# Performance work log

Measured on AMD Instinct MI355X. Metric: run time of the kernel, lower is better.

Reference implementation:

```python
import jax, jax.numpy as jnp
import numpy as np

EXPAND = 2
KCONV = 4


def _mamba(x, Win, Wconv, bconv, Wx, Wdt, bdt, Alog, Dskip, Wout):
    # x: (B, C, H, W) -> flatten HW to a sequence, run Mamba (S6) block, reshape back
    B, C, H, W = x.shape
    L = H * W
    Di, Kc = Wconv.shape
    R = Wdt.shape[0]
    N = Alog.shape[1]
    xl = x.reshape(B, C, L).transpose(0, 2, 1)            # (B, L, C)
    xz = xl @ Win                                          # (B, L, 2*Di)
    xs, z = xz[..., :Di], xz[..., Di:]
    xt = xs.transpose(0, 2, 1)                             # (B, Di, L)
    xp = jnp.pad(xt, ((0, 0), (0, 0), (Kc - 1, 0)))        # causal depthwise conv1d
    conv = bconv[None, :, None]
    for k in range(Kc):
        conv = conv + Wconv[:, k][None, :, None] * xp[:, :, k:k + L]
    u = jax.nn.silu(conv).transpose(0, 2, 1)               # (B, L, Di)
    dbc = u @ Wx                                           # (B, L, R+2N)
    dt = jax.nn.softplus(dbc[..., :R] @ Wdt + bdt)         # (B, L, Di)
    Bm = dbc[..., R:R + N]                                 # (B, L, N)
    Cm = dbc[..., R + N:]                                  # (B, L, N)
    A = -jnp.exp(Alog)                                     # (Di, N)
    dA = jnp.exp(dt[..., None] * A)                        # (B, L, Di, N)
    dBx = dt[..., None] * Bm[:, :, None, :] * u[..., None] # (B, L, Di, N)

    def step(h, inp):
        a, bx, c = inp
        h = a * h + bx
        return h, jnp.einsum('bdn,bn->bd', h, c)

    h0 = jnp.zeros((B, Di, N), x.dtype)
    _, ys = jax.lax.scan(step, h0, (jnp.swapaxes(dA, 0, 1), jnp.swapaxes(dBx, 0, 1), jnp.swapaxes(Cm, 0, 1)))
    y = jnp.swapaxes(ys, 0, 1) + u * Dskip                 # (B, L, Di)
    y = y * jax.nn.silu(z)
    return (y @ Wout).transpose(0, 2, 1).reshape(B, C, H, W)


def _resize_bilinear(x, oh, ow):
    # F.interpolate(mode='bilinear', align_corners=True)
    B, C, H, W = x.shape
    ys = jnp.linspace(0.0, H - 1.0, oh)
    xs = jnp.linspace(0.0, W - 1.0, ow)
    y0 = jnp.floor(ys).astype(jnp.int32); y1 = jnp.clip(y0 + 1, 0, H - 1); wy = (ys - y0)[:, None]
    x0 = jnp.floor(xs).astype(jnp.int32); x1 = jnp.clip(x0 + 1, 0, W - 1); wx = (xs - x0)[None, :]
    r0 = x[:, :, y0, :]
    r1 = x[:, :, y1, :]
    top = r0[..., x0] * (1 - wx) + r0[..., x1] * wx
    bot = r1[..., x0] * (1 - wx) + r1[..., x1] * wx
    return top * (1 - wy) + bot * wy


def _mamba_params(key, D, N):
    Di = EXPAND * D
    R = max(1, D // 16)
    ks = jax.random.split(key, 6)
    s = 0.02
    Win = s * jax.random.normal(ks[0], (D, 2 * Di), jnp.float32)
    Wconv = s * jax.random.normal(ks[1], (Di, KCONV), jnp.float32)
    bconv = jnp.zeros((Di,), jnp.float32)
    Wx = s * jax.random.normal(ks[2], (Di, R + 2 * N), jnp.float32)
    Wdt = s * jax.random.normal(ks[3], (R, Di), jnp.float32)
    bdt = s * jax.random.normal(ks[4], (Di,), jnp.float32)
    Alog = jnp.tile(jnp.log(jnp.arange(1, N + 1, dtype=jnp.float32))[None, :], (Di, 1))
    Dskip = jnp.ones((Di,), jnp.float32)
    Wout = s * jax.random.normal(ks[5], (Di, D), jnp.float32)
    return Win, Wconv, bconv, Wx, Wdt, bdt, Alog, Dskip, Wout


def setup_inputs() -> dict:
    key = jax.random.key(0)
    C, B, N = 64, 2, 16
    sizes = [48, 24, 12, 6]
    ks = jax.random.split(key, 16)
    inp = {}
    for i, s in enumerate(sizes):
        inp[f'feat{i}'] = jax.random.normal(ks[i], (B, C, s, s), jnp.float32)
    names = ['Win', 'Wconv', 'bconv', 'Wx', 'Wdt', 'bdt', 'Alog', 'D', 'Wout']
    lvl = [_mamba_params(ks[4 + i], C, N) for i in range(4)]
    for j, nm in enumerate(names):
        inp['lvl_' + nm] = jnp.stack([lvl[i][j] for i in range(4)])
    cr = _mamba_params(ks[8], 4 * C, N)
    for j, nm in enumerate(names):
        inp['cr_' + nm] = cr[j]
    inp['proj_W'] = 0.02 * jax.random.normal(ks[9], (C, 4 * C), jnp.float32)  # 1x1 conv weight (out,in)
    inp['proj_b'] = jnp.zeros((C,), jnp.float32)
    inp['bn_g'] = jnp.ones((C,), jnp.float32)
    inp['bn_b'] = jnp.zeros((C,), jnp.float32)
    inp['bn_m'] = 0.1 * jax.random.normal(ks[10], (C,), jnp.float32)
    inp['bn_v'] = jax.random.uniform(ks[11], (C,), jnp.float32, minval=0.5, maxval=1.5)
    inp['target_h'] = 48
    inp['target_w'] = 48
    return inp


def reference(feat0, feat1, feat2, feat3,
              lvl_Win, lvl_Wconv, lvl_bconv, lvl_Wx, lvl_Wdt, lvl_bdt, lvl_Alog, lvl_D, lvl_Wout,
              cr_Win, cr_Wconv, cr_bconv, cr_Wx, cr_Wdt, cr_bdt, cr_Alog, cr_D, cr_Wout,
              proj_W, proj_b, bn_g, bn_b, bn_m, bn_v, target_h, target_w):
    feats = [feat0, feat1, feat2, feat3]
    processed = []
    for i, f in enumerate(feats):
        f = f + _mamba(f, lvl_Win[i], lvl_Wconv[i], lvl_bconv[i], lvl_Wx[i], lvl_Wdt[i],
                       lvl_bdt[i], lvl_Alog[i], lvl_D[i], lvl_Wout[i])
        processed.append(_resize_bilinear(f, target_h, target_w))
    x = jnp.concatenate(processed, axis=1)                 # (B, 4C, th, tw)
    x = x + _mamba(x, cr_Win, cr_Wconv, cr_bconv, cr_Wx, cr_Wdt, cr_bdt, cr_Alog, cr_D, cr_Wout)
    y = jnp.einsum('bchw,oc->bohw', x, proj_W) + proj_b[None, :, None, None]
    scale = (bn_g / jnp.sqrt(bn_v + 1e-5))[None, :, None, None]
    y = (y - bn_m[None, :, None, None]) * scale + bn_b[None, :, None, None]
    return jax.nn.relu(y)
```

## Files before the change

### kernel.cpp

```cpp
#include <hip/hip_runtime.h>
#include <cmath>

#define DEV __device__ __forceinline__

typedef unsigned short u16;
typedef u16 u16x8 __attribute__((ext_vector_type(8)));
typedef u16 u16x4 __attribute__((ext_vector_type(4)));
typedef short bf16x8 __attribute__((ext_vector_type(8)));
typedef float f32x4 __attribute__((ext_vector_type(4)));

constexpr int B_ = 2;
constexpr int S4[4]    = {48, 24, 12, 6};
constexpr int L4[4]    = {2304, 576, 144, 36};
constexpr int LOFF4[4] = {0, 2304, 2880, 3024};
constexpr int LTOT = 3060;
constexpr int TOFF4[4] = {0, 144, 180, 189};
constexpr int NTT = 192;
constexpr int NCH4[4]   = {36, 9, 3, 1};
constexpr int CHOFF4[4] = {0, 36, 45, 48};
constexpr int NCHL = 49;
constexpr int NCHC = 36;
constexpr int LC = 2304;
constexpr float LOG2E = 1.44269504088896f;

DEV float siluf(float x) { return x / (1.f + __expf(-x)); }
DEV float softplusf(float x) { return fmaxf(x, 0.f) + log1pf(__expf(-fabsf(x))); }
DEV float b2f(u16 x) { union { float f; unsigned u; } v; v.u = ((unsigned)x) << 16; return v.f; }
DEV u16 f2b(float f) {
  union { float f; unsigned u; } v; v.f = f;
  unsigned r = v.u + 0x7fffu + ((v.u >> 16) & 1u);
  return (u16)(r >> 16);
}

__global__ __launch_bounds__(256) void k_prep(
    const float* __restrict__ projW, const float* __restrict__ crWout,
    const float* __restrict__ cWin, const float* __restrict__ cWx,
    float* __restrict__ Wt, float* __restrict__ WP,
    u16* __restrict__ WinT, float* __restrict__ WxT) {
  __shared__ float sm[64 * 65];
  int blk = blockIdx.x;
  int tid = threadIdx.x;
  if (blk < 64) {
    int i = blk * 256 + tid;
    int o = i >> 8, c = i & 255;
    Wt[c * 64 + o] = projW[o * 256 + c];
  } else if (blk < 192) {
    int i = (blk - 64) * 256 + tid;
    int d = i >> 6, o = i & 63;
    float acc = 0.f;
#pragma unroll 4
    for (int c = 0; c < 256; ++c)
      acc = fmaf(crWout[d * 256 + c], projW[o * 256 + c], acc);
    WP[d * 64 + o] = acc;
  } else if (blk < 256) {
    int t = blk - 192;
    int ct = t & 3, nt = t >> 2;
    int c0 = ct * 64, n0 = nt * 64;
    for (int i = tid; i < 4096; i += 256) {
      int cc = i >> 6, nn = i & 63;
      sm[cc * 65 + nn] = cWin[(size_t)(c0 + cc) * 1024 + n0 + nn];
    }
    __syncthreads();
    for (int i = tid; i < 4096; i += 256) {
      int nn = i >> 6, cc = i & 63;
      WinT[(size_t)(n0 + nn) * 256 + c0 + cc] = f2b(sm[cc * 65 + nn]);
    }
  } else {
    int i = (blk - 256) * 256 + tid;
    int d = i & 511, j = i >> 9;
    WxT[j * 512 + d] = cWx[d * 48 + j];
  }
}

__global__ __launch_bounds__(256) void k_front_lvl(
    const float* __restrict__ f0, const float* __restrict__ f1,
    const float* __restrict__ f2, const float* __restrict__ f3,
    const float* __restrict__ Win,
    const float* __restrict__ Wconv,
    const float* __restrict__ bconv,
    const float* __restrict__ Wx,
    const float* __restrict__ Wdt,
    const float* __restrict__ bdt,
    u16* __restrict__ u_l, u16* __restrict__ dt_l,
    u16* __restrict__ Bm_l, u16* __restrict__ Cm_l, u16* __restrict__ z_l) {
  __shared__ float s_x[64 * 20];
  __shared__ float s_xs[19 * 128];
  __shared__ float s_u[16 * 132];
  __shared__ float s_dbc[16 * 36];
  int bid = blockIdx.x;
  int b = bid / NTT, t = bid - b * NTT;
  int lvl = 0;
  while (lvl < 3 && t >= TOFF4[lvl + 1]) ++lvl;
  int tl = t - TOFF4[lvl];
  int L = L4[lvl], loff = LOFF4[lvl];
  int l0 = tl * 16;
  int nl = min(16, L - l0);
  const float* fx = lvl == 0 ? f0 : lvl == 1 ? f1 : lvl == 2 ? f2 : f3;
  int tid = threadIdx.x;

  for (int i = tid; i < 64 * 20; i += 256) {
    int c = i / 20, r = i - c * 20;
    int l = l0 - 3 + r;
    float v = 0.f;
    if (r < 19 && l >= 0 && l < L) v = fx[(size_t)(b * 64 + c) * L + l];
    s_x[i] = v;
  }
  __syncthreads();
  {
    int j = tid;
    float acc[19];
#pragma unroll
    for (int r = 0; r < 19; ++r) acc[r] = 0.f;
    const float* W = Win + lvl * 64 * 256 + j;
    for (int c = 0; c < 64; ++c) {
      float w = W[c * 256];
#pragma unroll
      for (int r = 0; r < 19; ++r) acc[r] = fmaf(w, s_x[c * 20 + r], acc[r]);
    }
    if (j < 128) {
#pragma unroll
      for (int r = 0; r < 19; ++r) s_xs[r * 128 + j] = acc[r];
    } else {
      int d = j - 128;
      int dti = d >> 4, jj = d & 15;
      for (int r = 3; r < 19; ++r) {
        int l = l0 - 3 + r;
        if (l < l0 + nl)
          z_l[((size_t)(b * 8 + dti) * LTOT + loff + l) * 16 + jj] = f2b(acc[r]);
      }
    }
  }
  __syncthreads();
  for (int i = tid; i < 16 * 128; i += 256) {
    int l = i >> 7, d = i & 127;
    if (l < nl) {
      const float* wc = Wconv + (lvl * 128 + d) * 4;
      float a = bconv[lvl * 128 + d];
#pragma unroll
      for (int k = 0; k < 4; ++k) a = fmaf(wc[k], s_xs[(l + k) * 128 + d], a);
      float uu = siluf(a);
      s_u[l * 132 + d] = uu;
      u_l[((size_t)(b * 8 + (d >> 4)) * LTOT + loff + l0 + l) * 16 + (d & 15)] = f2b(uu);
    }
  }
  __syncthreads();
  for (int i = tid; i < 16 * 36; i += 256) {
    int l = i & 15, jj = i >> 4;
    if (l < nl) {
      const float* wx = Wx + lvl * 128 * 36 + jj;
      float a = 0.f;
      for (int d = 0; d < 128; ++d) a = fmaf(s_u[l * 132 + d], wx[d * 36], a);
      s_dbc[l * 36 + jj] = a;
      if (jj >= 4) {
        int q = jj - 4;
        size_t gb = ((size_t)(b * LTOT) + loff + l0 + l) * 16;
        if (q < 16) Bm_l[gb + q] = f2b(a);
        else        Cm_l[gb + (q - 16)] = f2b(a);
      }
    }
  }
  __syncthreads();
  for (int i = tid; i < 16 * 128; i += 256) {
    int l = i >> 7, d = i & 127;
    if (l < nl) {
      float a = bdt[lvl * 128 + d];
#pragma unroll
      for (int r = 0; r < 4; ++r)
        a = fmaf(s_dbc[l * 36 + r], Wdt[(lvl * 4 + r) * 128 + d], a);
      dt_l[((size_t)(b * 8 + (d >> 4)) * LTOT + loff + l0 + l) * 16 + (d & 15)] =
          f2b(softplusf(a));
    }
  }
}

template <int MODE, int PASSC>
__global__ __launch_bounds__(256) void k_scan(
    const u16* __restrict__ dtb, const u16* __restrict__ ub,
    const u16* __restrict__ Bmb, const u16* __restrict__ Cmb,
    const u16* __restrict__ zb,
    const float* __restrict__ Alog, const float* __restrict__ Dsk,
    float* __restrict__ hloc, float* __restrict__ Ssum,
    const float* __restrict__ hin, u16* __restrict__ yg) {
  constexpr int DI = MODE ? 512 : 128;
  constexpr int NDT = DI / 16;
  constexpr int NB = DI / 64;
  constexpr int NCHT = MODE ? NCHC : NCHL;
  constexpr int LT = MODE ? LC : LTOT;
  __shared__ __align__(16) u16 smem[PASSC ? 14336 : 9216];
  u16* s_dt = smem;
  u16* s_u  = smem + 4096;
  u16* s_B  = smem + 8192;
  u16* s_C  = PASSC ? smem + 9216 : nullptr;
  u16* s_y  = PASSC ? smem + 10240 : nullptr;

  int bid = blockIdx.x;
  int dblk = bid % NB;
  int rem = bid / NB;
  int gc = rem % NCHT;
  int b = rem / NCHT;
  int lvl = 0, ch = gc, Lq = LC, loff = 0;
  if (MODE == 0) {
    while (lvl < 3 && gc >= CHOFF4[lvl + 1]) ++lvl;
    ch = gc - CHOFF4[lvl];
    Lq = L4[lvl];
    loff = LOFF4[lvl];
  }
  int l0 = ch * 64;
  int len = min(64, Lq - l0);
  int labs0 = loff + l0;
  int tid = threadIdx.x;
  int q = tid & 3;
  int dl = (tid >> 2) & 15;
  int ti_l = tid >> 6;
  int dti = dblk * 4 + ti_l;
  int d = dti * 16 + dl;
  int n0 = q * 4;

  for (int ti = 0; ti < 4; ++ti) {
    size_t g2 = ((size_t)(b * NDT + dblk * 4 + ti) * LT + labs0) * 16;
    const u16x8* pdt = (const u16x8*)(dtb + g2);
    const u16x8* pu  = (const u16x8*)(ub + g2);
    for (int i = tid; i < len * 2; i += 256) {
      *(u16x8*)&s_dt[ti * 1024 + i * 8] = pdt[i];
      *(u16x8*)&s_u [ti * 1024 + i * 8] = pu[i];
    }
  }
  {
    size_t gB = ((size_t)b * LT + labs0) * 16;
    for (int i = tid; i < len * 2; i += 256) {
      *(u16x8*)&s_B[i * 8] = *(const u16x8*)&Bmb[gB + i * 8];
      if (PASSC) *(u16x8*)&s_C[i * 8] = *(const u16x8*)&Cmb[gB + i * 8];
    }
  }
  __syncthreads();

  int ai = (MODE ? d : lvl * 128 + d);
  float4 al = *(const float4*)&Alog[ai * 16 + n0];
  float kA2[4] = {-__expf(al.x) * LOG2E, -__expf(al.y) * LOG2E,
                  -__expf(al.z) * LOG2E, -__expf(al.w) * LOG2E};
  size_t hix = (((size_t)(b * NCHT) + gc) * DI + d) * 16 + n0;
  float h[4] = {0.f, 0.f, 0.f, 0.f};
  if (PASSC) {
    float4 hv = *(const float4*)&hin[hix];
    h[0] = hv.x; h[1] = hv.y; h[2] = hv.z; h[3] = hv.w;
  }
  float dsk = PASSC ? Dsk[ai] : 0.f;
  float ss = 0.f;

  for (int l = 0; l < len; ++l) {
    float dt = b2f(s_dt[ti_l * 1024 + l * 16 + dl]);
    float uu = b2f(s_u [ti_l * 1024 + l * 16 + dl]);
    float dtu = dt * uu;
    u16x4 Bv = *(const u16x4*)&s_B[l * 16 + n0];
    if (PASSC) {
      u16x4 Cv = *(const u16x4*)&s_C[l * 16 + n0];
      float p = 0.f;
#pragma unroll
      for (int i = 0; i < 4; ++i) {
        float dA = exp2f(kA2[i] * dt);
        h[i] = fmaf(dA, h[i], dtu * b2f(Bv[i]));
        p = fmaf(h[i], b2f(Cv[i]), p);
      }
      p += __shfl_xor(p, 1, 4);
      p += __shfl_xor(p, 2, 4);
      if (q == 0) s_y[l * 64 + ti_l * 16 + dl] = f2b(fmaf(uu, dsk, p));
    } else {
#pragma unroll
      for (int i = 0; i < 4; ++i) {
        float dA = exp2f(kA2[i] * dt);
        h[i] = fmaf(dA, h[i], dtu * b2f(Bv[i]));
      }
      ss += dt;
    }
  }
  if (!PASSC) {
    f32x4 hv = {h[0], h[1], h[2], h[3]};
    *(f32x4*)&hloc[hix] = hv;
    if (q == 0) Ssum[((size_t)(b * NCHT) + gc) * DI + d] = ss;
  } else {
    __syncthreads();
    for (int ti = 0; ti < 4; ++ti) {
      size_t g2 = ((size_t)(b * NDT + dblk * 4 + ti) * LT + labs0) * 16;
      for (int i = tid; i < len * 2; i += 256) {
        u16x8 zv = *(const u16x8*)&zb[g2 + i * 8];
        u16x8 yv = *(const u16x8*)&s_y[(i >> 1) * 64 + ti * 16 + (i & 1) * 8];
        u16x8 o;
#pragma unroll
        for (int j = 0; j < 8; ++j) {
          float z = b2f(zv[j]);
          float gate = z / (1.f + __expf(-z));
          o[j] = f2b(b2f(yv[j]) * gate);
        }
        *(u16x8*)&yg[g2 + i * 8] = o;
      }
    }
  }
}

__global__ __launch_bounds__(256) void k_combine_lvl(
    const float* __restrict__ Alog, const float* __restrict__ hloc,
    const float* __restrict__ Ssum, float* __restrict__ hin) {
  int i = blockIdx.x * 256 + threadIdx.x;
  int n = i & 15, d = (i >> 4) & 127, lvl = (i >> 11) & 3, b = i >> 13;
  float kA2 = -__expf(Alog[(lvl * 128 + d) * 16 + n]) * LOG2E;
  float h = 0.f;
  int nch = NCH4[lvl];
  for (int ch = 0; ch < nch; ++ch) {
    int gc = CHOFF4[lvl] + ch;
    size_t ix = (((size_t)(b * NCHL) + gc) * 128 + d) * 16 + n;
    hin[ix] = h;
    float S = Ssum[((size_t)(b * NCHL) + gc) * 128 + d];
    h = fmaf(exp2f(kA2 * S), h, hloc[ix]);
  }
}

__global__ __launch_bounds__(256) void k_combine_cr(
    const float* __restrict__ Alog, const float* __restrict__ hloc,
    const float* __restrict__ Ssum, float* __restrict__ hin) {
  int i = blockIdx.x * 256 + threadIdx.x;
  int n = i & 15, d = (i >> 4) & 511, b = i >> 13;
  float kA2 = -__expf(Alog[d * 16 + n]) * LOG2E;
  float h = 0.f;
  for (int ch = 0; ch < NCHC; ++ch) {
    size_t ix = (((size_t)(b * NCHC) + ch) * 512 + d) * 16 + n;
    hin[ix] = h;
    float S = Ssum[((size_t)(b * NCHC) + ch) * 512 + d];
    h = fmaf(exp2f(kA2 * S), h, hloc[ix]);
  }
}

__global__ __launch_bounds__(256) void k_out_lvl(
    const u16* __restrict__ yg_l, const float* __restrict__ Wout,
    const float* __restrict__ f0, const float* __restrict__ f1,
    const float* __restrict__ f2, const float* __restrict__ f3,
    float* __restrict__ fout) {
  __shared__ float s_ygT[128 * 20];
  __shared__ float s_o[16 * 64];
  int bid = blockIdx.x;
  int b = bid / NTT, t = bid - b * NTT;
  int lvl = 0;
  while (lvl < 3 && t >= TOFF4[lvl + 1]) ++lvl;
  int tl = t - TOFF4[lvl];
  int L = L4[lvl], loff = LOFF4[lvl];
  int l0 = tl * 16, nl = min(16, L - l0);
  const float* fx = lvl == 0 ? f0 : lvl == 1 ? f1 : lvl == 2 ? f2 : f3;
  int tid = threadIdx.x;
  for (int i = tid; i < 16 * 128; i += 256) {
    int d = i & 127, l = i >> 7;
    float v = 0.f;
    if (l < nl)
      v = b2f(yg_l[((size_t)(b * 8 + (d >> 4)) * LTOT + loff + l0 + l) * 16 + (d & 15)]);
    s_ygT[d * 20 + l] = v;
  }
  __syncthreads();
  {
    int c = tid & 63, lg = (tid >> 6) * 4;
    float acc[4] = {0.f, 0.f, 0.f, 0.f};
    const float* W = Wout + lvl * 128 * 64 + c;
    for (int dq = 0; dq < 128; ++dq) {
      float w = W[dq * 64];
      float4 yv = *(const float4*)&s_ygT[dq * 20 + lg];
      acc[0] = fmaf(w, yv.x, acc[0]);
      acc[1] = fmaf(w, yv.y, acc[1]);
      acc[2] = fmaf(w, yv.z, acc[2]);
      acc[3] = fmaf(w, yv.w, acc[3]);
    }
#pragma unroll
    for (int a = 0; a < 4; ++a) s_o[(lg + a) * 64 + c] = acc[a];
  }
  __syncthreads();
  for (int i = tid; i < 16 * 64; i += 256) {
    int c = i >> 4, l = i & 15;
    if (l < nl)
      fout[((size_t)(b * 64) + c) * LTOT + loff + l0 + l] =
          s_o[l * 64 + c] + fx[((size_t)(b * 64) + c) * L + l0 + l];
  }
}

__global__ __launch_bounds__(256) void k_resize(const float* __restrict__ fout,
                                                float* __restrict__ xTf,
                                                u16* __restrict__ xTb) {
  int i = blockIdx.x * 256 + threadIdx.x;
  int ch = i & 255;
  int rem = i >> 8;
  int hw = rem % 2304;
  int b = rem / 2304;
  int oh = hw / 48, ow = hw - oh * 48;
  int lvl = ch >> 6, c = ch & 63;
  int s = S4[lvl];
  const float* base = fout + ((size_t)(b * 64) + c) * LTOT + LOFF4[lvl];
  float scl = (float)(s - 1) * (1.f / 47.f);
  float fy = oh * scl, fxx = ow * scl;
  int y0 = (int)floorf(fy), x0 = (int)floorf(fxx);
  float wy = fy - y0, wx = fxx - x0;
  int y1 = min(y0 + 1, s - 1), x1 = min(x0 + 1, s - 1);
  float v00 = base[y0 * s + x0], v01 = base[y0 * s + x1];
  float v10 = base[y1 * s + x0], v11 = base[y1 * s + x1];
  float top = v00 * (1.f - wx) + v01 * wx;
  float bot = v10 * (1.f - wx) + v11 * wx;
  float v = top * (1.f - wy) + bot * wy;
  xTf[i] = v;
  xTb[i] = f2b(v);
}

__global__ __launch_bounds__(256) void k_gemm_mfma(
    const u16* __restrict__ xT,
    const u16* __restrict__ WT,
    u16* __restrict__ xs_c, u16* __restrict__ z_c) {
  __shared__ __align__(16) u16 s_a[64 * 72];
  __shared__ __align__(16) u16 s_b[128 * 72];
  int bid = blockIdx.x;
  int nj = bid & 7, bm = bid >> 3;
  int tid = threadIdx.x;
  int lane = tid & 63, w = tid >> 6;
  int wm = (w & 1) * 32, wn = (w >> 1) * 64;
  const int m_base = bm * 64;
  const int n_base = nj * 128;

  f32x4 acc[2][4];
#pragma unroll
  for (int mi = 0; mi < 2; ++mi)
#pragma unroll
    for (int ni = 0; ni < 4; ++ni) acc[mi][ni] = {0.f, 0.f, 0.f, 0.f};

  u16x8 ra0, ra1, rb0, rb1, rb2, rb3;
  auto ld = [&](int c0) {
#pragma unroll
    for (int s = 0; s < 2; ++s) {
      int v = s * 256 + tid;
      int row = v >> 3, kc = (v & 7) * 8;
      u16x8 t = *(const u16x8*)&xT[(size_t)(m_base + row) * 256 + c0 + kc];
      if (s == 0) ra0 = t; else ra1 = t;
    }
#pragma unroll
    for (int s = 0; s < 4; ++s) {
      int v = s * 256 + tid;
      int row = v >> 3, kc = (v & 7) * 8;
      u16x8 t = *(const u16x8*)&WT[(size_t)(n_base + row) * 256 + c0 + kc];
      if (s == 0) rb0 = t; else if (s == 1) rb1 = t;
      else if (s == 2) rb2 = t; else rb3 = t;
    }
  };
  auto st = [&]() {
#pragma unroll
    for (int s = 0; s < 2; ++s) {
      int v = s * 256 + tid;
      int row = v >> 3, kc = (v & 7) * 8;
      *(u16x8*)&s_a[row * 72 + kc] = (s == 0) ? ra0 : ra1;
    }
#pragma unroll
    for (int s = 0; s < 4; ++s) {
      int v = s * 256 + tid;
      int row = v >> 3, kc = (v & 7) * 8;
      const u16x8& t = (s == 0) ? rb0 : (s == 1) ? rb1 : (s == 2) ? rb2 : rb3;
      *(u16x8*)&s_b[row * 72 + kc] = t;
    }
  };
  ld(0);
  int mlane = lane & 15, kg = (lane >> 4) * 8;
  for (int kt = 0; kt < 4; ++kt) {
    st();
    __syncthreads();
    if (kt < 3) ld((kt + 1) * 64);
#pragma unroll
    for (int kk = 0; kk < 2; ++kk) {
      int k0 = kk * 32 + kg;
      bf16x8 af[2], bfr[4];
#pragma unroll
      for (int mi = 0; mi < 2; ++mi)
        af[mi] = *(const bf16x8*)&s_a[(wm + mi * 16 + mlane) * 72 + k0];
#pragma unroll
      for (int ni = 0; ni < 4; ++ni)
        bfr[ni] = *(const bf16x8*)&s_b[(wn + ni * 16 + mlane) * 72 + k0];
#pragma unroll
      for (int mi = 0; mi < 2; ++mi)
#pragma unroll
        for (int ni = 0; ni < 4; ++ni)
          acc[mi][ni] = __builtin_amdgcn_mfma_f32_16x16x32_bf16(
              af[mi], bfr[ni], acc[mi][ni], 0, 0, 0);
    }
    __syncthreads();
  }
  int rgrp = (lane >> 4) * 4;
#pragma unroll
  for (int mi = 0; mi < 2; ++mi) {
#pragma unroll
    for (int ni = 0; ni < 4; ++ni) {
      int n = n_base + wn + ni * 16 + mlane;
#pragma unroll
      for (int r = 0; r < 4; ++r) {
        int gm = m_base + wm + mi * 16 + rgrp + r;
        int b = gm >= 2304;
        int l = gm - b * 2304;
        u16 v = f2b(acc[mi][ni][r]);
        if (n < 512) {
          xs_c[((size_t)(b * LC) + l) * 512 + n] = v;
        } else {
          int dz = n - 512;
          z_c[((size_t)(b * 32 + (dz >> 4)) * LC + l) * 16 + (dz & 15)] = v;
        }
      }
    }
  }
}

__global__ __launch_bounds__(256) void k_mid_cr(
    const u16* __restrict__ xs_c,
    const float* __restrict__ Wconv,
    const float* __restrict__ bconv,
    const float* __restrict__ WxT,
    const float* __restrict__ Wdt,
    const float* __restrict__ bdt, u16* __restrict__ u_c,
    u16* __restrict__ dt_c, u16* __restrict__ Bm_c, u16* __restrict__ Cm_c) {
  __shared__ __align__(16) u16 s_xs[11 * 512];
  __shared__ __align__(16) float s_u[8 * 516];
  __shared__ float s_dbc[8 * 48];
  int bid = blockIdx.x;
  int b = bid / 288, tl = bid - b * 288;
  int l0 = tl * 8;
  int tid = threadIdx.x;
  for (int i = tid; i < 704; i += 256) {
    int r = i >> 6;
    int l = l0 - 3 + r;
    u16x8 v = {0, 0, 0, 0, 0, 0, 0, 0};
    if (l >= 0)
      v = *(const u16x8*)&xs_c[((size_t)(b * LC) + l) * 512 + (i & 63) * 8];
    *(u16x8*)&s_xs[i * 8] = v;
  }
  __syncthreads();
  for (int i = tid; i < 8 * 512; i += 256) {
    int l = i >> 9, d = i & 511;
    const float* wc = Wconv + d * 4;
    float a = bconv[d];
#pragma unroll
    for (int k = 0; k < 4; ++k) a = fmaf(wc[k], b2f(s_xs[(l + k) * 512 + d]), a);
    float uu = siluf(a);
    s_u[l * 516 + d] = uu;
    u_c[((size_t)(b * 32 + (d >> 4)) * LC + l0 + l) * 16 + (d & 15)] = f2b(uu);
  }
  __syncthreads();
  for (int i = tid; i < 8 * 48; i += 256) {
    int jj = i >> 3, l = i & 7;
    const float* wx = WxT + jj * 512;
    float a = 0.f;
#pragma unroll 4
    for (int d = 0; d < 512; d += 4) {
      float4 w4 = *(const float4*)&wx[d];
      float4 u4 = *(const float4*)&s_u[l * 516 + d];
      a = fmaf(w4.x, u4.x, a);
      a = fmaf(w4.y, u4.y, a);
      a = fmaf(w4.z, u4.z, a);
      a = fmaf(w4.w, u4.w, a);
    }
    s_dbc[l * 48 + jj] = a;
    if (jj >= 16) {
      int q = jj - 16;
      size_t gb = ((size_t)(b * LC) + l0 + l) * 16;
      if (q < 16) Bm_c[gb + q] = f2b(a);
      else        Cm_c[gb + (q - 16)] = f2b(a);
    }
  }
  __syncthreads();
  for (int i = tid; i < 8 * 512; i += 256) {
    int l = i >> 9, d = i & 511;
    float a = bdt[d];
#pragma unroll
    for (int r = 0; r < 16; ++r)
      a = fmaf(s_dbc[l * 48 + r], Wdt[r * 512 + d], a);
    dt_c[((size_t)(b * 32 + (d >> 4)) * LC + l0 + l) * 16 + (d & 15)] =
        f2b(softplusf(a));
  }
}

__global__ __launch_bounds__(256) void k_final(
    const float* __restrict__ xTf, const u16* __restrict__ yg_c,
    const float* __restrict__ Wt, const float* __restrict__ WP,
    const float* __restrict__ pb, const float* __restrict__ bng,
    const float* __restrict__ bnb, const float* __restrict__ bnm,
    const float* __restrict__ bnv, float* __restrict__ out) {
  __shared__ float s_xc[256 * 8];
  __shared__ float s_yg[512 * 8];
  __shared__ float s_w[32 * 64];
  int bid = blockIdx.x;
  int b = bid / 288, tl = bid - b * 288;
  int l0 = tl * 8;
  int tid = threadIdx.x;
  for (int i = tid; i < 2048; i += 256) {
    int c = i & 255, l = i >> 8;
    s_xc[c * 8 + l] = xTf[((size_t)(b * 2304) + l0 + l) * 256 + c];
  }
  for (int i = tid; i < 4096; i += 256) {
    int j = i & 15, l = (i >> 4) & 7, dt = i >> 7;
    s_yg[(dt * 16 + j) * 8 + l] =
        b2f(yg_c[((size_t)(b * 32 + dt) * LC + l0 + l) * 16 + j]);
  }
  int o = tid & 63, lg = (tid >> 6) * 2;
  float acc0 = 0.f, acc1 = 0.f;
  float4 r0, r1;
  auto ldT = [&](const float* W, int kt, float4& a0, float4& a1) {
#pragma unroll
    for (int s = 0; s < 2; ++s) {
      int idx = s * 256 + tid;
      int row = idx >> 4, c4 = (idx & 15) << 2;
      float4 v = *(const float4*)&W[(kt * 32 + row) * 64 + c4];
      if (s == 0) a0 = v; else a1 = v;
    }
  };
  auto stT = [&](const float4& a0, const float4& a1) {
#pragma unroll
    for (int s = 0; s < 2; ++s) {
      int idx = s * 256 + tid;
      int row = idx >> 4, c4 = (idx & 15) << 2;
      *(float4*)&s_w[row * 64 + c4] = (s == 0) ? a0 : a1;
    }
  };
  ldT(Wt, 0, r0, r1);
  __syncthreads();
  stT(r0, r1);
  __syncthreads();
  for (int kt = 0; kt < 8; ++kt) {
    if (kt < 7) ldT(Wt, kt + 1, r0, r1);
    else ldT(WP, 0, r0, r1);
#pragma unroll
    for (int cc = 0; cc < 32; ++cc) {
      float w = s_w[cc * 64 + o];
      float2 xv = *(const float2*)&s_xc[(kt * 32 + cc) * 8 + lg];
      acc0 = fmaf(w, xv.x, acc0);
      acc1 = fmaf(w, xv.y, acc1);
    }
    __syncthreads();
    stT(r0, r1);
    __syncthreads();
  }
  for (int kt = 0; kt < 16; ++kt) {
    if (kt < 15) ldT(WP, kt + 1, r0, r1);
#pragma unroll
    for (int cc = 0; cc < 32; ++cc) {
      float w = s_w[cc * 64 + o];
      float2 yv = *(const float2*)&s_yg[(kt * 32 + cc) * 8 + lg];
      acc0 = fmaf(w, yv.x, acc0);
      acc1 = fmaf(w, yv.y, acc1);
    }
    __syncthreads();
    if (kt < 15) {
      stT(r0, r1);
      __syncthreads();
    }
  }
  float bias = pb[o], m = bnm[o], g = bng[o], v = bnv[o], bb = bnb[o];
  float scl = g * (1.f / sqrtf(v + 1e-5f));
  float2 r;
  r.x = fmaxf((acc0 + bias - m) * scl + bb, 0.f);
  r.y = fmaxf((acc1 + bias - m) * scl + bb, 0.f);
  *(float2*)&out[((size_t)(b * 64) + o) * LC + l0 + lg] = r;
}

extern "C" void kernel_launch(void* const* d_in, const int* in_sizes, int n_in,
                              void* d_out, int out_size, void* d_ws,
                              size_t ws_size, hipStream_t stream) {
  (void)in_sizes; (void)n_in; (void)out_size; (void)ws_size;
  const float* f0 = (const float*)d_in[0];
  const float* f1 = (const float*)d_in[1];
  const float* f2 = (const float*)d_in[2];
  const float* f3 = (const float*)d_in[3];
  const float* lWin   = (const float*)d_in[4];
  const float* lWconv = (const float*)d_in[5];
  const float* lbconv = (const float*)d_in[6];
  const float* lWx    = (const float*)d_in[7];
  const float* lWdt   = (const float*)d_in[8];
  const float* lbdt   = (const float*)d_in[9];
  const float* lAlog  = (const float*)d_in[10];
  const float* lD     = (const float*)d_in[11];
  const float* lWout  = (const float*)d_in[12];
  const float* cWin   = (const float*)d_in[13];
  const float* cWconv = (const float*)d_in[14];
  const float* cbconv = (const float*)d_in[15];
  const float* cWx    = (const float*)d_in[16];
  const float* cWdt   = (const float*)d_in[17];
  const float* cbdt   = (const float*)d_in[18];
  const float* cAlog  = (const float*)d_in[19];
  const float* cD     = (const float*)d_in[20];
  const float* cWout  = (const float*)d_in[21];
  const float* projW  = (const float*)d_in[22];
  const float* projb  = (const float*)d_in[23];
  const float* bng    = (const float*)d_in[24];
  const float* bnb    = (const float*)d_in[25];
  const float* bnm    = (const float*)d_in[26];
  const float* bnv    = (const float*)d_in[27];
  float* out = (float*)d_out;

  float* ws = (float*)d_ws;
  size_t off = 0;
  auto allocf = [&](size_t n) { float* p = ws + off; off += (n + 7) & ~(size_t)7; return p; };
  auto allocb = [&](size_t n) { u16* p = (u16*)(ws + off); off += ((n + 1) / 2 + 7) & ~(size_t)7; return p; };

  float* Wt     = allocf(256 * 64);
  float* WP     = allocf(512 * 64);
  float* WxT    = allocf(48 * 512);
  float* fout   = allocf((size_t)B_ * 64 * LTOT);
  float* xTf    = allocf((size_t)B_ * LC * 256);
  float* hloc_l = allocf((size_t)B_ * NCHL * 128 * 16);
  float* S_l    = allocf((size_t)B_ * NCHL * 128);
  float* hin_l  = allocf((size_t)B_ * NCHL * 128 * 16);
  float* hloc_c = allocf((size_t)B_ * NCHC * 512 * 16);
  float* S_c    = allocf((size_t)B_ * NCHC * 512);
  float* hin_c  = allocf((size_t)B_ * NCHC * 512 * 16);

  u16* WinT  = allocb(1024 * 256);
  u16* xTb   = allocb((size_t)B_ * LC * 256);
  u16* u_l2  = allocb((size_t)B_ * 8 * LTOT * 16);
  u16* dt_l2 = allocb((size_t)B_ * 8 * LTOT * 16);
  u16* z_l2  = allocb((size_t)B_ * 8 * LTOT * 16);
  u16* yg_l2 = allocb((size_t)B_ * 8 * LTOT * 16);
  u16* Bm_l2 = allocb((size_t)B_ * LTOT * 16);
  u16* Cm_l2 = allocb((size_t)B_ * LTOT * 16);
  u16* xs_c2 = allocb((size_t)B_ * LC * 512);
  u16* u_c2  = allocb((size_t)B_ * 32 * LC * 16);
  u16* dt_c2 = allocb((size_t)B_ * 32 * LC * 16);
  u16* z_c2  = allocb((size_t)B_ * 32 * LC * 16);
  u16* yg_c2 = allocb((size_t)B_ * 32 * LC * 16);
  u16* Bm_c2 = allocb((size_t)B_ * LC * 16);
  u16* Cm_c2 = allocb((size_t)B_ * LC * 16);

  k_prep<<<352, 256, 0, stream>>>(projW, cWout, cWin, cWx, Wt, WP, WinT, WxT);

  k_front_lvl<<<B_ * NTT, 256, 0, stream>>>(f0, f1, f2, f3, lWin, lWconv,
                                            lbconv, lWx, lWdt, lbdt, u_l2,
                                            dt_l2, Bm_l2, Cm_l2, z_l2);

  k_scan<0, 0><<<B_ * NCHL * 2, 256, 0, stream>>>(
      dt_l2, u_l2, Bm_l2, Cm_l2, nullptr, lAlog, lD, hloc_l, S_l, nullptr,
      nullptr);
  k_combine_lvl<<<64, 256, 0, stream>>>(lAlog, hloc_l, S_l, hin_l);
  k_scan<0, 1><<<B_ * NCHL * 2, 256, 0, stream>>>(
      dt_l2, u_l2, Bm_l2, Cm_l2, z_l2, lAlog, lD, nullptr, nullptr, hin_l,
      yg_l2);

  k_out_lvl<<<B_ * NTT, 256, 0, stream>>>(yg_l2, lWout, f0, f1, f2, f3, fout);
  k_resize<<<(B_ * 256 * LC) / 256, 256, 0, stream>>>(fout, xTf, xTb);

  k_gemm_mfma<<<72 * 8, 256, 0, stream>>>(xTb, WinT, xs_c2, z_c2);
  k_mid_cr<<<B_ * 288, 256, 0, stream>>>(xs_c2, cWconv, cbconv, WxT, cWdt,
                                         cbdt, u_c2, dt_c2, Bm_c2, Cm_c2);

  k_scan<1, 0><<<B_ * NCHC * 8, 256, 0, stream>>>(
      dt_c2, u_c2, Bm_c2, Cm_c2, nullptr, cAlog, cD, hloc_c, S_c, nullptr,
      nullptr);
  k_combine_cr<<<64, 256, 0, stream>>>(cAlog, hloc_c, S_c, hin_c);
  k_scan<1, 1><<<B_ * NCHC * 8, 256, 0, stream>>>(
      dt_c2, u_c2, Bm_c2, Cm_c2, z_c2, cAlog, cD, nullptr, nullptr, hin_c,
      yg_c2);

  k_final<<<B_ * 288, 256, 0, stream>>>(xTf, yg_c2, Wt, WP, projb, bng, bnb,
                                        bnm, bnv, out);
}
```

Baseline: 350.6 us.

## Retile cross-level mid kernel: 16 positions per block, LDS-staged Wx projection

```diff
diff --git a/kernel.cpp b/kernel.cpp
--- a/kernel.cpp
+++ b/kernel.cpp
@@ -504,7 +504,7 @@
   }
 }
 
-__global__ __launch_bounds__(256) void k_mid_cr(
+__global__ __launch_bounds__(1024) void k_mid_cr(
     const u16* __restrict__ xs_c,
     const float* __restrict__ Wconv,
     const float* __restrict__ bconv,
@@ -512,56 +512,76 @@
     const float* __restrict__ Wdt,
     const float* __restrict__ bdt, u16* __restrict__ u_c,
     u16* __restrict__ dt_c, u16* __restrict__ Bm_c, u16* __restrict__ Cm_c) {
-  __shared__ __align__(16) u16 s_xs[11 * 512];
-  __shared__ __align__(16) float s_u[8 * 516];
-  __shared__ float s_dbc[8 * 48];
+  __shared__ __align__(16) u16 s_xs[19 * 512];
+  __shared__ __align__(16) u16 s_ub[16 * 520];
+  __shared__ __align__(16) float s_wx[48 * 132];
+  __shared__ float s_dbc[16 * 48];
   int bid = blockIdx.x;
-  int b = bid / 288, tl = bid - b * 288;
-  int l0 = tl * 8;
+  int b = bid / 144, tl = bid - b * 144;
+  int l0 = tl * 16;
   int tid = threadIdx.x;
-  for (int i = tid; i < 704; i += 256) {
-    int r = i >> 6;
+  for (int i = tid; i < 19 * 64; i += 1024) {
+    int r = i >> 6, c8 = (i & 63) * 8;
     int l = l0 - 3 + r;
     u16x8 v = {0, 0, 0, 0, 0, 0, 0, 0};
     if (l >= 0)
-      v = *(const u16x8*)&xs_c[((size_t)(b * LC) + l) * 512 + (i & 63) * 8];
-    *(u16x8*)&s_xs[i * 8] = v;
-  }
-  __syncthreads();
-  for (int i = tid; i < 8 * 512; i += 256) {
+      v = *(const u16x8*)&xs_c[((size_t)(b * LC) + l) * 512 + c8];
+    *(u16x8*)&s_xs[r * 512 + c8] = v;
+  }
+  __syncthreads();
+  for (int i = tid; i < 16 * 512; i += 1024) {
     int l = i >> 9, d = i & 511;
     const float* wc = Wconv + d * 4;
     float a = bconv[d];
 #pragma unroll
     for (int k = 0; k < 4; ++k) a = fmaf(wc[k], b2f(s_xs[(l + k) * 512 + d]), a);
     float uu = siluf(a);
-    s_u[l * 516 + d] = uu;
-    u_c[((size_t)(b * 32 + (d >> 4)) * LC + l0 + l) * 16 + (d & 15)] = f2b(uu);
-  }
-  __syncthreads();
-  for (int i = tid; i < 8 * 48; i += 256) {
-    int jj = i >> 3, l = i & 7;
-    const float* wx = WxT + jj * 512;
-    float a = 0.f;
+    u16 ub = f2b(uu);
+    s_ub[l * 520 + d] = ub;
+    u_c[((size_t)(b * 32 + (d >> 4)) * LC + l0 + l) * 16 + (d & 15)] = ub;
+  }
+  int dl = tid & 15, jj = tid >> 4;
+  float a8[8] = {0.f, 0.f, 0.f, 0.f, 0.f, 0.f, 0.f, 0.f};
+  for (int kt = 0; kt < 4; ++kt) {
+    __syncthreads();
+    for (int i = tid; i < 1536; i += 1024) {
+      int row = i >> 5, c4 = (i & 31) * 4;
+      *(float4*)&s_wx[row * 132 + c4] =
+          *(const float4*)&WxT[row * 512 + kt * 128 + c4];
+    }
+    __syncthreads();
+    if (tid < 768) {
+      const u16* ur = s_ub + dl * 520 + kt * 128;
+      const float* wr = s_wx + jj * 132;
 #pragma unroll 4
-    for (int d = 0; d < 512; d += 4) {
-      float4 w4 = *(const float4*)&wx[d];
-      float4 u4 = *(const float4*)&s_u[l * 516 + d];
-      a = fmaf(w4.x, u4.x, a);
-      a = fmaf(w4.y, u4.y, a);
-      a = fmaf(w4.z, u4.z, a);
-      a = fmaf(w4.w, u4.w, a);
-    }
-    s_dbc[l * 48 + jj] = a;
+      for (int kb = 0; kb < 16; ++kb) {
+        u16x8 uv = *(const u16x8*)&ur[kb * 8];
+        float4 w0 = *(const float4*)&wr[kb * 8];
+        float4 w1 = *(const float4*)&wr[kb * 8 + 4];
+        a8[0] = fmaf(b2f(uv[0]), w0.x, a8[0]);
+        a8[1] = fmaf(b2f(uv[1]), w0.y, a8[1]);
+        a8[2] = fmaf(b2f(uv[2]), w0.z, a8[2]);
+        a8[3] = fmaf(b2f(uv[3]), w0.w, a8[3]);
+        a8[4] = fmaf(b2f(uv[4]), w1.x, a8[4]);
+        a8[5] = fmaf(b2f(uv[5]), w1.y, a8[5]);
+        a8[6] = fmaf(b2f(uv[6]), w1.z, a8[6]);
+        a8[7] = fmaf(b2f(uv[7]), w1.w, a8[7]);
+      }
+    }
+  }
+  if (tid < 768) {
+    float a = ((a8[0] + a8[1]) + (a8[2] + a8[3])) +
+              ((a8[4] + a8[5]) + (a8[6] + a8[7]));
+    s_dbc[dl * 48 + jj] = a;
     if (jj >= 16) {
       int q = jj - 16;
-      size_t gb = ((size_t)(b * LC) + l0 + l) * 16;
+      size_t gb = ((size_t)(b * LC) + l0 + dl) * 16;
       if (q < 16) Bm_c[gb + q] = f2b(a);
       else        Cm_c[gb + (q - 16)] = f2b(a);
     }
   }
   __syncthreads();
-  for (int i = tid; i < 8 * 512; i += 256) {
+  for (int i = tid; i < 16 * 512; i += 1024) {
     int l = i >> 9, d = i & 511;
     float a = bdt[d];
 #pragma unroll
@@ -740,8 +760,8 @@
   k_resize<<<(B_ * 256 * LC) / 256, 256, 0, stream>>>(fout, xTf, xTb);
 
   k_gemm_mfma<<<72 * 8, 256, 0, stream>>>(xTb, WinT, xs_c2, z_c2);
-  k_mid_cr<<<B_ * 288, 256, 0, stream>>>(xs_c2, cWconv, cbconv, WxT, cWdt,
-                                         cbdt, u_c2, dt_c2, Bm_c2, Cm_c2);
+  k_mid_cr<<<B_ * 144, 1024, 0, stream>>>(xs_c2, cWconv, cbconv, WxT, cWdt,
+                                          cbdt, u_c2, dt_c2, Bm_c2, Cm_c2);
 
   k_scan<1, 0><<<B_ * NCHC * 8, 256, 0, stream>>>(
       dt_c2, u_c2, Bm_c2, Cm_c2, nullptr, cAlog, cD, hloc_c, S_c, nullptr,
```

New measurement: 342.9 us. -2.2%, faster.
